# Kernel tuning notes

Hardware: AMD Instinct MI355X
Metric: run time of the kernel (lower is better)

The kernel has to match this reference:

```python
import jax, jax.numpy as jnp
import numpy as np

B, S, D, H = 32, 4096, 128, 8

def setup_inputs() -> dict:
    key = jax.random.key(0)
    kx, kkq, kv = jax.random.split(key, 3)
    x = jax.random.normal(kx, (B, S, D), dtype=jnp.float32)
    # nn.Linear weights: y = x @ W.T, weight shape [D, D]; stacked over heads.
    W_kq = jax.random.normal(kkq, (H, D, D), dtype=jnp.float32)
    W_v = jax.random.normal(kv, (H, D, D), dtype=jnp.float32)
    return {"x": x, "W_kq": W_kq, "W_v": W_v}


def reference(x, W_kq, W_v):
    # Original per-head math:
    #   kq_h = x @ W_kq[h].T                      [B,S,D]
    #   scores_h = x @ kq_h^T = x @ W_kq[h] @ x^T [B,S,S]
    #   out_h = scores_h @ (x @ W_v[h].T)
    # Reassociated (identical math, linear in S):
    #   out = x @ (sum_h W_kq[h] @ (x^T x) @ W_v[h].T)
    G = jnp.einsum('bsd,bse->bde', x, x)              # [B,D,D] = x^T x
    M = jnp.einsum('hde,bef,hgf->bdg', W_kq, G, W_v)  # sum over heads h
    out = jnp.einsum('bsd,bdg->bsg', x, M)            # [B,S,D]
    return out
```

## Files before the change

kernel.cpp:

```cpp
#include <hip/hip_runtime.h>
#include <hip/hip_bf16.h>

#define BB 32
#define SS 4096
#define DD 128
#define HH 8

typedef __attribute__((ext_vector_type(8))) short short8;
typedef __attribute__((ext_vector_type(4))) float f32x4;
typedef unsigned long long u64;

__device__ inline unsigned short f2b(float f){
  unsigned int u = __float_as_uint(f);
  return (unsigned short)((u + 0x7fffu + ((u >> 16) & 1u)) >> 16);
}

__device__ inline int swzi(int r, int c){
  return (r << 7) | (((c >> 3) ^ (r & 7)) << 3) | (c & 7);
}

__device__ inline short8 ldfrag(const short* buf, int row, int kblk){
  return *reinterpret_cast<const short8*>(&buf[(row << 7) | ((kblk ^ (row & 7)) << 3)]);
}

__device__ inline short8 ldxfrag(const float* __restrict__ base, int row, int kblk){
  const float4* p = reinterpret_cast<const float4*>(base) + row * 32 + kblk * 2;
  float4 a = p[0], b = p[1];
  short8 r;
  r[0] = (short)f2b(a.x); r[1] = (short)f2b(a.y); r[2] = (short)f2b(a.z); r[3] = (short)f2b(a.w);
  r[4] = (short)f2b(b.x); r[5] = (short)f2b(b.y); r[6] = (short)f2b(b.z); r[7] = (short)f2b(b.w);
  return r;
}

__device__ inline void wave_gemm32x64(const short* bufA, const short* bufB,
                                      int wm, int wn, int lane, f32x4 acc[2][4]){
  #pragma unroll
  for (int ks = 0; ks < 4; ++ks){
    int kblk = ks * 4 + (lane >> 4);
    short8 af[2], bf[4];
    #pragma unroll
    for (int mt = 0; mt < 2; ++mt) af[mt] = ldfrag(bufA, wm + mt * 16 + (lane & 15), kblk);
    #pragma unroll
    for (int nt = 0; nt < 4; ++nt) bf[nt] = ldfrag(bufB, wn + nt * 16 + (lane & 15), kblk);
    #pragma unroll
    for (int mt = 0; mt < 2; ++mt)
      #pragma unroll
      for (int nt = 0; nt < 4; ++nt)
        acc[mt][nt] = __builtin_amdgcn_mfma_f32_16x16x32_bf16(af[mt], bf[nt], acc[mt][nt], 0, 0, 0);
  }
}

__device__ inline void wave_gemm32x32(const short* bufA, const short* bufB,
                                      int wm, int wn, int lane, f32x4 acc[2][2]){
  #pragma unroll
  for (int ks = 0; ks < 4; ++ks){
    int kblk = ks * 4 + (lane >> 4);
    short8 af[2], bf[2];
    #pragma unroll
    for (int mt = 0; mt < 2; ++mt) af[mt] = ldfrag(bufA, wm + mt * 16 + (lane & 15), kblk);
    #pragma unroll
    for (int nt = 0; nt < 2; ++nt) bf[nt] = ldfrag(bufB, wn + nt * 16 + (lane & 15), kblk);
    #pragma unroll
    for (int mt = 0; mt < 2; ++mt)
      #pragma unroll
      for (int nt = 0; nt < 2; ++nt)
        acc[mt][nt] = __builtin_amdgcn_mfma_f32_16x16x32_bf16(af[mt], bf[nt], acc[mt][nt], 0, 0, 0);
  }
}

__device__ inline u64 packb4(float a, float b, float c, float d){
  return (u64)f2b(a) | ((u64)f2b(b) << 16) | ((u64)f2b(c) << 32) | ((u64)f2b(d) << 48);
}

template<int R>
__device__ inline void stageR(const float* __restrict__ src, short* dst, int t){
  const float4* s4 = reinterpret_cast<const float4*>(src);
  #pragma unroll
  for (int f4 = t; f4 < R * 32; f4 += 512){
    int r = f4 >> 5, c = (f4 & 31) << 2;
    float4 v = s4[f4];
    *reinterpret_cast<u64*>(&dst[swzi(r, c)]) = packb4(v.x, v.y, v.z, v.w);
  }
}

__device__ inline void ld128(const float* __restrict__ src, int t, float4 r[8]){
  const float4* s4 = reinterpret_cast<const float4*>(src);
  #pragma unroll
  for (int i = 0; i < 8; ++i) r[i] = s4[t + i * 512];
}
__device__ inline void wr128(short* dst, int t, const float4 r[8]){
  #pragma unroll
  for (int i = 0; i < 8; ++i){
    int f4 = t + i * 512;
    int rr = f4 >> 5, c = (f4 & 31) << 2;
    *reinterpret_cast<u64*>(&dst[swzi(rr, c)]) = packb4(r[i].x, r[i].y, r[i].z, r[i].w);
  }
}

__global__ __launch_bounds__(512) void k_gram(const float* __restrict__ x, float* __restrict__ Gp){
  __shared__ short xsT[128 * 128];
  const int t = threadIdx.x, lane = t & 63, wid = t >> 6;
  const int slot = blockIdx.x, b = blockIdx.y;
  const int e = t & 127, sb0 = t >> 7;
  const int wm = (wid >> 1) * 32, wn = (wid & 1) * 64;

  f32x4 acc[2][4];
  const f32x4 z = {0.f, 0.f, 0.f, 0.f};
  #pragma unroll
  for (int i = 0; i < 2; ++i)
    #pragma unroll
    for (int j = 0; j < 4; ++j) acc[i][j] = z;

  const float* xb = x + ((size_t)b * SS + slot * 512) * DD;
  float v[4][8];
  #pragma unroll
  for (int i = 0; i < 4; ++i)
    #pragma unroll
    for (int j = 0; j < 8; ++j)
      v[i][j] = xb[(size_t)(((sb0 + 4 * i) * 8 + j)) * DD + e];

  for (int c = 0; c < 4; ++c){
    __syncthreads();
    #pragma unroll
    for (int i = 0; i < 4; ++i){
      int sb = sb0 + 4 * i;
      short8 w;
      #pragma unroll
      for (int j = 0; j < 8; ++j) w[j] = (short)f2b(v[i][j]);
      *reinterpret_cast<short8*>(&xsT[(e << 7) | ((sb ^ (e & 7)) << 3)]) = w;
    }
    if (c < 3){
      const float* src = xb + (size_t)(c + 1) * 128 * DD;
      #pragma unroll
      for (int i = 0; i < 4; ++i)
        #pragma unroll
        for (int j = 0; j < 8; ++j)
          v[i][j] = src[(size_t)(((sb0 + 4 * i) * 8 + j)) * DD + e];
    }
    __syncthreads();
    wave_gemm32x64(xsT, xsT, wm, wn, lane, acc);
  }

  float* Gb = Gp + (size_t)(slot * BB + b) * (DD * DD);
  #pragma unroll
  for (int mt = 0; mt < 2; ++mt)
    #pragma unroll
    for (int nt = 0; nt < 4; ++nt)
      #pragma unroll
      for (int i = 0; i < 4; ++i){
        int ee = wm + mt * 16 + ((lane >> 4) << 2) + i;
        int ff = wn + nt * 16 + (lane & 15);
        Gb[(ee << 7) + ff] = acc[mt][nt][i];
      }
}

__global__ __launch_bounds__(256) void k_gsum(const float* __restrict__ Gp, short* __restrict__ Gbf){
  const int id = blockIdx.x * 256 + threadIdx.x;
  const float4* g4 = reinterpret_cast<const float4*>(Gp);
  #pragma unroll
  for (int it = 0; it < 4; ++it){
    int F = id + it * 32768;
    int b = F >> 12, j4 = F & 4095;
    float4 s = {0.f, 0.f, 0.f, 0.f};
    #pragma unroll
    for (int sl = 0; sl < 8; ++sl){
      float4 vv = g4[(size_t)(sl * BB + b) * 4096 + j4];
      s.x += vv.x; s.y += vv.y; s.z += vv.z; s.w += vv.w;
    }
    int r = j4 >> 5, c = (j4 & 31) << 2;
    *reinterpret_cast<u64*>(&Gbf[(size_t)b * 16384 + swzi(r, c)]) = packb4(s.x, s.y, s.z, s.w);
  }
}

__global__ __launch_bounds__(512) void k_heads(const short* __restrict__ Gbf,
                                               const float* __restrict__ Wkq,
                                               const float* __restrict__ Wv,
                                               float* __restrict__ Mp){
  __shared__ short bufA[64 * 128];
  __shared__ short bufB[128 * 128];
  const int t = threadIdx.x, lane = t & 63, wid = t >> 6;
  const int h = blockIdx.x >> 1, gh = blockIdx.x & 1, b = blockIdx.y;
  const int wm = (wid >> 2) * 32, wn = (wid & 3) * 32;
  const f32x4 z = {0.f, 0.f, 0.f, 0.f};

  stageR<64>(Wv + (size_t)h * DD * DD + (size_t)gh * 64 * DD, bufA, t);
  {
    const short8* g8 = reinterpret_cast<const short8*>(Gbf + (size_t)b * 16384);
    short8* d8 = reinterpret_cast<short8*>(bufB);
    #pragma unroll
    for (int i = 0; i < 4; ++i) d8[t + i * 512] = g8[t + i * 512];
  }
  __syncthreads();

  float4 wk[8];
  ld128(Wkq + (size_t)h * DD * DD, t, wk);

  f32x4 acc[2][2];
  #pragma unroll
  for (int i = 0; i < 2; ++i)
    #pragma unroll
    for (int j = 0; j < 2; ++j) acc[i][j] = z;
  wave_gemm32x32(bufA, bufB, wm, wn, lane, acc);
  __syncthreads();

  #pragma unroll
  for (int mt = 0; mt < 2; ++mt)
    #pragma unroll
    for (int nt = 0; nt < 2; ++nt)
      #pragma unroll
      for (int i = 0; i < 4; ++i){
        int g = wm + mt * 16 + ((lane >> 4) << 2) + i;
        int e = wn + nt * 16 + (lane & 15);
        bufA[swzi(g, e)] = (short)f2b(acc[mt][nt][i]);
      }
  wr128(bufB, t, wk);
  __syncthreads();

  #pragma unroll
  for (int i = 0; i < 2; ++i)
    #pragma unroll
    for (int j = 0; j < 2; ++j) acc[i][j] = z;
  wave_gemm32x32(bufA, bufB, wm, wn, lane, acc);

  float* Mb = Mp + (size_t)(h * BB + b) * (DD * DD) + (size_t)gh * 64 * DD;
  #pragma unroll
  for (int mt = 0; mt < 2; ++mt)
    #pragma unroll
    for (int nt = 0; nt < 2; ++nt)
      #pragma unroll
      for (int i = 0; i < 4; ++i){
        int g = wm + mt * 16 + ((lane >> 4) << 2) + i;
        int d = wn + nt * 16 + (lane & 15);
        Mb[(g << 7) + d] = acc[mt][nt][i];
      }
}

__global__ __launch_bounds__(256) void k_red(const float* __restrict__ Mp, short* __restrict__ Mb){
  const int id = blockIdx.x * 256 + threadIdx.x;
  const float4* p4 = reinterpret_cast<const float4*>(Mp);
  u64* o8 = reinterpret_cast<u64*>(Mb);
  #pragma unroll
  for (int it = 0; it < 4; ++it){
    int F = id + it * 32768;
    int b = F >> 12, j4 = F & 4095;
    float4 s = {0.f, 0.f, 0.f, 0.f};
    #pragma unroll
    for (int hh = 0; hh < 8; ++hh){
      float4 vv = p4[(size_t)(hh * BB + b) * 4096 + j4];
      s.x += vv.x; s.y += vv.y; s.z += vv.z; s.w += vv.w;
    }
    o8[F] = packb4(s.x, s.y, s.z, s.w);
  }
}

__global__ __launch_bounds__(512) void k_out(const float* __restrict__ x,
                                             const short* __restrict__ Mbf,
                                             float* __restrict__ out){
  __shared__ short bufM[128 * 128];
  const int t = threadIdx.x, lane = t & 63, wid = t >> 6;
  const int b = blockIdx.y, s0 = blockIdx.x * 256;
  const int wm = (wid >> 1) * 32, wn = (wid & 1) * 64;
  const f32x4 z = {0.f, 0.f, 0.f, 0.f};

  {
    const short8* m8 = reinterpret_cast<const short8*>(Mbf + (size_t)b * DD * DD);
    #pragma unroll
    for (int i = 0; i < 4; ++i){
      int idx = t + i * 512;
      int r = idx >> 4, c8 = idx & 15;
      *reinterpret_cast<short8*>(&bufM[(r << 7) | ((c8 ^ (r & 7)) << 3)]) = m8[idx];
    }
  }
  __syncthreads();

  const float* xb = x + ((size_t)b * SS + s0) * DD;
  #pragma unroll
  for (int c = 0; c < 2; ++c){
    f32x4 acc[2][4];
    #pragma unroll
    for (int i = 0; i < 2; ++i)
      #pragma unroll
      for (int j = 0; j < 4; ++j) acc[i][j] = z;

    #pragma unroll
    for (int ks = 0; ks < 4; ++ks){
      int kblk = ks * 4 + (lane >> 4);
      short8 af[2], bf[4];
      #pragma unroll
      for (int mt = 0; mt < 2; ++mt)
        af[mt] = ldxfrag(xb, c * 128 + wm + mt * 16 + (lane & 15), kblk);
      #pragma unroll
      for (int nt = 0; nt < 4; ++nt) bf[nt] = ldfrag(bufM, wn + nt * 16 + (lane & 15), kblk);
      #pragma unroll
      for (int mt = 0; mt < 2; ++mt)
        #pragma unroll
        for (int nt = 0; nt < 4; ++nt)
          acc[mt][nt] = __builtin_amdgcn_mfma_f32_16x16x32_bf16(af[mt], bf[nt], acc[mt][nt], 0, 0, 0);
    }

    float* ob = out + ((size_t)b * SS + s0 + c * 128) * DD;
    #pragma unroll
    for (int mt = 0; mt < 2; ++mt)
      #pragma unroll
      for (int nt = 0; nt < 4; ++nt)
        #pragma unroll
        for (int i = 0; i < 4; ++i){
          int sp = wm + mt * 16 + ((lane >> 4) << 2) + i;
          int g = wn + nt * 16 + (lane & 15);
          ob[(sp << 7) + g] = acc[mt][nt][i];
        }
  }
}

extern "C" void kernel_launch(void* const* d_in, const int* in_sizes, int n_in,
                              void* d_out, int out_size, void* d_ws, size_t ws_size,
                              hipStream_t stream) {
  const float* x   = (const float*)d_in[0];
  const float* Wkq = (const float*)d_in[1];
  const float* Wv  = (const float*)d_in[2];
  float* out = (float*)d_out;

  float* Gp  = (float*)d_ws;
  float* Mp  = Gp + (size_t)8 * BB * DD * DD;
  short* Gbf = (short*)(Mp + (size_t)HH * BB * DD * DD);
  short* Mb  = Gbf + (size_t)BB * DD * DD;

  k_gram <<<dim3(8, BB),        512, 0, stream>>>(x, Gp);
  k_gsum <<<dim3(128),          256, 0, stream>>>(Gp, Gbf);
  k_heads<<<dim3(2 * HH, BB),   512, 0, stream>>>(Gbf, Wkq, Wv, Mp);
  k_red  <<<dim3(128),          256, 0, stream>>>(Mp, Mb);
  k_out  <<<dim3(SS / 256, BB), 512, 0, stream>>>(x, Mb, out);
}
```

Before: 149.8 us.

## Replace split-K reduction kernels with atomicAdd into zeroed fp32 buffers

```diff
diff --git a/kernel.cpp b/kernel.cpp
--- a/kernel.cpp
+++ b/kernel.cpp
@@ -97,7 +97,7 @@
   }
 }
 
-__global__ __launch_bounds__(512) void k_gram(const float* __restrict__ x, float* __restrict__ Gp){
+__global__ __launch_bounds__(512) void k_gram(const float* __restrict__ x, float* __restrict__ Gf){
   __shared__ short xsT[128 * 128];
   const int t = threadIdx.x, lane = t & 63, wid = t >> 6;
   const int slot = blockIdx.x, b = blockIdx.y;
@@ -141,7 +141,7 @@
     wave_gemm32x64(xsT, xsT, wm, wn, lane, acc);
   }
 
-  float* Gb = Gp + (size_t)(slot * BB + b) * (DD * DD);
+  float* Gb = Gf + (size_t)b * (DD * DD);
   #pragma unroll
   for (int mt = 0; mt < 2; ++mt)
     #pragma unroll
@@ -150,32 +150,14 @@
       for (int i = 0; i < 4; ++i){
         int ee = wm + mt * 16 + ((lane >> 4) << 2) + i;
         int ff = wn + nt * 16 + (lane & 15);
-        Gb[(ee << 7) + ff] = acc[mt][nt][i];
+        atomicAdd(&Gb[(ee << 7) + ff], acc[mt][nt][i]);
       }
 }
 
-__global__ __launch_bounds__(256) void k_gsum(const float* __restrict__ Gp, short* __restrict__ Gbf){
-  const int id = blockIdx.x * 256 + threadIdx.x;
-  const float4* g4 = reinterpret_cast<const float4*>(Gp);
-  #pragma unroll
-  for (int it = 0; it < 4; ++it){
-    int F = id + it * 32768;
-    int b = F >> 12, j4 = F & 4095;
-    float4 s = {0.f, 0.f, 0.f, 0.f};
-    #pragma unroll
-    for (int sl = 0; sl < 8; ++sl){
-      float4 vv = g4[(size_t)(sl * BB + b) * 4096 + j4];
-      s.x += vv.x; s.y += vv.y; s.z += vv.z; s.w += vv.w;
-    }
-    int r = j4 >> 5, c = (j4 & 31) << 2;
-    *reinterpret_cast<u64*>(&Gbf[(size_t)b * 16384 + swzi(r, c)]) = packb4(s.x, s.y, s.z, s.w);
-  }
-}
-
-__global__ __launch_bounds__(512) void k_heads(const short* __restrict__ Gbf,
+__global__ __launch_bounds__(512) void k_heads(const float* __restrict__ Gf,
                                                const float* __restrict__ Wkq,
                                                const float* __restrict__ Wv,
-                                               float* __restrict__ Mp){
+                                               float* __restrict__ Mf){
   __shared__ short bufA[64 * 128];
   __shared__ short bufB[128 * 128];
   const int t = threadIdx.x, lane = t & 63, wid = t >> 6;
@@ -184,12 +166,7 @@
   const f32x4 z = {0.f, 0.f, 0.f, 0.f};
 
   stageR<64>(Wv + (size_t)h * DD * DD + (size_t)gh * 64 * DD, bufA, t);
-  {
-    const short8* g8 = reinterpret_cast<const short8*>(Gbf + (size_t)b * 16384);
-    short8* d8 = reinterpret_cast<short8*>(bufB);
-    #pragma unroll
-    for (int i = 0; i < 4; ++i) d8[t + i * 512] = g8[t + i * 512];
-  }
+  stageR<128>(Gf + (size_t)b * DD * DD, bufB, t);
   __syncthreads();
 
   float4 wk[8];
@@ -222,7 +199,7 @@
     for (int j = 0; j < 2; ++j) acc[i][j] = z;
   wave_gemm32x32(bufA, bufB, wm, wn, lane, acc);
 
-  float* Mb = Mp + (size_t)(h * BB + b) * (DD * DD) + (size_t)gh * 64 * DD;
+  float* Mb = Mf + (size_t)b * (DD * DD) + (size_t)gh * 64 * DD;
   #pragma unroll
   for (int mt = 0; mt < 2; ++mt)
     #pragma unroll
@@ -231,30 +208,12 @@
       for (int i = 0; i < 4; ++i){
         int g = wm + mt * 16 + ((lane >> 4) << 2) + i;
         int d = wn + nt * 16 + (lane & 15);
-        Mb[(g << 7) + d] = acc[mt][nt][i];
+        atomicAdd(&Mb[(g << 7) + d], acc[mt][nt][i]);
       }
 }
 
-__global__ __launch_bounds__(256) void k_red(const float* __restrict__ Mp, short* __restrict__ Mb){
-  const int id = blockIdx.x * 256 + threadIdx.x;
-  const float4* p4 = reinterpret_cast<const float4*>(Mp);
-  u64* o8 = reinterpret_cast<u64*>(Mb);
-  #pragma unroll
-  for (int it = 0; it < 4; ++it){
-    int F = id + it * 32768;
-    int b = F >> 12, j4 = F & 4095;
-    float4 s = {0.f, 0.f, 0.f, 0.f};
-    #pragma unroll
-    for (int hh = 0; hh < 8; ++hh){
-      float4 vv = p4[(size_t)(hh * BB + b) * 4096 + j4];
-      s.x += vv.x; s.y += vv.y; s.z += vv.z; s.w += vv.w;
-    }
-    o8[F] = packb4(s.x, s.y, s.z, s.w);
-  }
-}
-
 __global__ __launch_bounds__(512) void k_out(const float* __restrict__ x,
-                                             const short* __restrict__ Mbf,
+                                             const float* __restrict__ Mf,
                                              float* __restrict__ out){
   __shared__ short bufM[128 * 128];
   const int t = threadIdx.x, lane = t & 63, wid = t >> 6;
@@ -262,15 +221,7 @@
   const int wm = (wid >> 1) * 32, wn = (wid & 1) * 64;
   const f32x4 z = {0.f, 0.f, 0.f, 0.f};
 
-  {
-    const short8* m8 = reinterpret_cast<const short8*>(Mbf + (size_t)b * DD * DD);
-    #pragma unroll
-    for (int i = 0; i < 4; ++i){
-      int idx = t + i * 512;
-      int r = idx >> 4, c8 = idx & 15;
-      *reinterpret_cast<short8*>(&bufM[(r << 7) | ((c8 ^ (r & 7)) << 3)]) = m8[idx];
-    }
-  }
+  stageR<128>(Mf + (size_t)b * DD * DD, bufM, t);
   __syncthreads();
 
   const float* xb = x + ((size_t)b * SS + s0) * DD;
@@ -320,14 +271,11 @@
   const float* Wv  = (const float*)d_in[2];
   float* out = (float*)d_out;
 
-  float* Gp  = (float*)d_ws;
-  float* Mp  = Gp + (size_t)8 * BB * DD * DD;
-  short* Gbf = (short*)(Mp + (size_t)HH * BB * DD * DD);
-  short* Mb  = Gbf + (size_t)BB * DD * DD;
-
-  k_gram <<<dim3(8, BB),        512, 0, stream>>>(x, Gp);
-  k_gsum <<<dim3(128),          256, 0, stream>>>(Gp, Gbf);
-  k_heads<<<dim3(2 * HH, BB),   512, 0, stream>>>(Gbf, Wkq, Wv, Mp);
-  k_red  <<<dim3(128),          256, 0, stream>>>(Mp, Mb);
-  k_out  <<<dim3(SS / 256, BB), 512, 0, stream>>>(x, Mb, out);
-}
+  float* Gf = (float*)d_ws;
+  float* Mf = Gf + (size_t)BB * DD * DD;
+
+  hipMemsetAsync(d_ws, 0, (size_t)2 * BB * DD * DD * sizeof(float), stream);
+  k_gram <<<dim3(8, BB),        512, 0, stream>>>(x, Gf);
+  k_heads<<<dim3(2 * HH, BB),   512, 0, stream>>>(Gf, Wkq, Wv, Mf);
+  k_out  <<<dim3(SS / 256, BB), 512, 0, stream>>>(x, Mf, out);
+}
```

After: 160.8 us. 7.3% more time.
